# Optimization experiments

Measured on AMD Instinct MI355X. Metric: run time of the kernel, lower is better.

## Reference

```python
import jax, jax.numpy as jnp
import numpy as np

K = 7      # kernel_size
PAD = 3    # padding ('same' with stride 1)
G = 16     # groups


def _unfold(x):
    """torch nn.Unfold equivalent, stride=1, dilation=1.
    Returns [B, C, K*K, H, W] with kernel positions ordered (kh, kw),
    matching torch's (c, kh, kw) channel-major layout after reshape."""
    B, C, H, W = x.shape
    xp = jnp.pad(x, ((0, 0), (0, 0), (PAD, PAD), (PAD, PAD)))
    patches = jnp.stack(
        [xp[:, :, i:i + H, j:j + W] for i in range(K) for j in range(K)],
        axis=2,
    )
    return patches


def setup_inputs() -> dict:
    key = jax.random.key(0)
    k1, k2, k3 = jax.random.split(key, 3)
    B, C, H, W = 4, 256, 64, 64
    x = jax.random.normal(k1, (B, C, H, W), dtype=jnp.float32)
    # 1x1 conv producing kernel_prod*groups = 49*16 = 784 channels (with bias)
    w_kernel = jax.random.normal(k2, (G * K * K, C), dtype=jnp.float32) * 0.05
    b_kernel = jax.random.normal(k3, (G * K * K,), dtype=jnp.float32) * 0.05
    return {"x": x, "w_kernel": w_kernel, "b_kernel": b_kernel}


def reference(x, w_kernel, b_kernel):
    B, C, H, W = x.shape
    Cg = C // G
    # unfolded input: [B, G, C//G, K*K, H, W]
    patches = _unfold(x).reshape(B, G, Cg, K * K, H, W)
    # dynamic per-pixel kernel: AvgPool(k=1) is identity at stride 1,
    # then 1x1 conv with bias -> [B, G*K*K, H, W]
    kern = jnp.einsum('bchw,kc->bkhw', x, w_kernel) + b_kernel[None, :, None, None]
    kern = kern.reshape(B, G, 1, K * K, H, W)
    # multiply and sum-reduce over kernel positions, flatten groups
    out = (patches * kern).sum(axis=3).reshape(B, C, H, W)
    return out
```

## Files before the change

kernel.cpp:

```cpp
#include <hip/hip_runtime.h>


#define B_   4
#define C_   256
#define G_   16
#define KK_  49
#define KS_  7
#define PD_  3

#define PROW  72
#define POCT  (70*PROW)
#define XP8_BYTES (B_*32*POCT*16)
#define WBF_OFF   XP8_BYTES

typedef __attribute__((ext_vector_type(8))) short bf16x8;
typedef __attribute__((ext_vector_type(4))) float f32x4;
typedef unsigned short ushort_t;

__device__ inline unsigned f2bf(float f) {
    unsigned u = __float_as_uint(f);
    u += 0x7FFF + ((u >> 16) & 1);
    return u >> 16;
}

__global__ __launch_bounds__(256)
void cvt_xp8(const float* __restrict__ x, const float* __restrict__ wk,
             ushort_t* __restrict__ xp8, unsigned* __restrict__ wbf) {
    const int t = threadIdx.x;
    if (blockIdx.x == 64) {
        const int slice = blockIdx.z * 4 + blockIdx.y;
        const float2* wk2 = (const float2*)wk;
        const int base = slice * 6272;
        for (int k = t; k < 6272; k += 256) {
            float2 v = wk2[base + k];
            wbf[base + k] = f2bf(v.x) | (f2bf(v.y) << 16);
        }
        return;
    }
    if (blockIdx.x == 65) {
        const int b  = blockIdx.z;
        const int o0 = blockIdx.y * 8;
        const uint4 z = make_uint4(0u, 0u, 0u, 0u);
        for (int e = t; e < 6 * PROW * 8; e += 256) {
            const int o = e / (6 * PROW);
            const int f = e - o * (6 * PROW);
            const int r = f / PROW;
            const int c = f - r * PROW;
            const int row = (r < 3) ? r : 64 + r;
            *(uint4*)(xp8 + ((size_t)((b << 5) + o0 + o) * POCT + row * PROW + c) * 8) = z;
        }
        return;
    }
    __shared__ float tile[64][65];
    const int c0 = blockIdx.y * 64;
    const int b  = blockIdx.z;
    const int px_r = t & 63;
    #pragma unroll
    for (int i = 0; i < 16; ++i) {
        int ch = (t >> 6) + i * 4;
        tile[ch][px_r] = x[((size_t)(b * C_ + c0 + ch) << 12) + blockIdx.x * 64 + px_r];
    }
    __syncthreads();
    const int lane = t & 63;
    const int ob = t >> 6;
    #pragma unroll
    for (int jj = 0; jj < 2; ++jj) {
        const int j = ob + jj * 4;
        ushort_t* rowbase = xp8 + ((size_t)((b << 5) + (c0 >> 3) + j) * POCT
                                   + (blockIdx.x + 3) * PROW) * 8;
        #pragma unroll
        for (int cc = 0; cc < 2; ++cc) {
            const int col = lane + cc * 64;
            if (col < PROW) {
                uint4 v = make_uint4(0u, 0u, 0u, 0u);
                if (col >= 3 && col < 67) {
                    const int p = col - 3;
                    unsigned u[4];
                    #pragma unroll
                    for (int k2 = 0; k2 < 4; ++k2) {
                        float a0 = tile[j * 8 + 2 * k2][p];
                        float a1 = tile[j * 8 + 2 * k2 + 1][p];
                        u[k2] = f2bf(a0) | (f2bf(a1) << 16);
                    }
                    v = make_uint4(u[0], u[1], u[2], u[3]);
                }
                *(uint4*)(rowbase + col * 8) = v;
            }
        }
    }
}

__global__ __launch_bounds__(512, 8)
void inv_fused(const ushort_t* __restrict__ xp8,
               const ushort_t* __restrict__ wbf,
               const float* __restrict__ bk,
               float* __restrict__ out) {
    __shared__ unsigned lds[7168];

    const int bid  = blockIdx.x;
    const int g    = bid >> 6;
    const int b    = (bid >> 4) & 3;
    const int tile = bid & 15;
    const int gy0  = tile * 4;
    const int p0   = tile * 256;

    const int tid  = threadIdx.x;
    const int wv   = tid >> 6;
    const int ln15 = tid & 15;
    const int quad = (tid & 63) >> 4;

    f32x4 acc[8];
    #pragma unroll
    for (int i = 0; i < 8; ++i) acc[i] = (f32x4){0.f, 0.f, 0.f, 0.f};

    const char* bbase = (const char*)xp8 + (size_t)b * 32 * POCT * 16;
    const char* abase = (const char*)wbf + (size_t)g * KK_ * 512;

    int vb0, vb1;
    {
        int gi0 = p0 + wv * 32 + ln15;
        int gi1 = gi0 + 16;
        vb0 = (quad * POCT + ((gi0 >> 6) + 3) * PROW + 3 + (gi0 & 63)) * 16;
        vb1 = (quad * POCT + ((gi1 >> 6) + 3) * PROW + 3 + (gi1 & 63)) * 16;
    }
    int va  = ln15 * 512 + quad * 16;
    const int va3 = 48 * 512 + quad * 16;

    #pragma unroll
    for (int k = 0; k < 8; ++k) {
        bf16x8 af0 = *(const bf16x8*)(abase + va);
        bf16x8 af1 = *(const bf16x8*)(abase + 8192 + va);
        bf16x8 af2 = *(const bf16x8*)(abase + 16384 + va);
        bf16x8 af3 = *(const bf16x8*)(abase + va3 + k * 64);
        bf16x8 bf0 = *(const bf16x8*)(bbase + vb0);
        bf16x8 bf1 = *(const bf16x8*)(bbase + vb1);
        acc[0] = __builtin_amdgcn_mfma_f32_16x16x32_bf16(af0, bf0, acc[0], 0, 0, 0);
        acc[1] = __builtin_amdgcn_mfma_f32_16x16x32_bf16(af0, bf1, acc[1], 0, 0, 0);
        acc[2] = __builtin_amdgcn_mfma_f32_16x16x32_bf16(af1, bf0, acc[2], 0, 0, 0);
        acc[3] = __builtin_amdgcn_mfma_f32_16x16x32_bf16(af1, bf1, acc[3], 0, 0, 0);
        acc[4] = __builtin_amdgcn_mfma_f32_16x16x32_bf16(af2, bf0, acc[4], 0, 0, 0);
        acc[5] = __builtin_amdgcn_mfma_f32_16x16x32_bf16(af2, bf1, acc[5], 0, 0, 0);
        acc[6] = __builtin_amdgcn_mfma_f32_16x16x32_bf16(af3, bf0, acc[6], 0, 0, 0);
        acc[7] = __builtin_amdgcn_mfma_f32_16x16x32_bf16(af3, bf1, acc[7], 0, 0, 0);
        va  += 64;
        vb0 += 4 * POCT * 16; vb1 += 4 * POCT * 16;
    }

    #define HALO_LD(e_) ({                                                     \
        int e = (e_);                                                          \
        int o = (e >= 700) ? 1 : 0;                                            \
        int f = e - o * 700;                                                   \
        int r = f / 70;                                                        \
        int c = f - r * 70;                                                    \
        *(const uint4*)(bbase + ((size_t)(2 * g + o) * POCT                    \
                                 + (gy0 + r) * PROW + c) * 16); })
    uint4 h0 = HALO_LD(tid);
    uint4 h1 = HALO_LD(tid + 512);
    uint4 h2 = (tid < 376) ? HALO_LD(tid + 1024) : make_uint4(0u, 0u, 0u, 0u);

    #pragma unroll
    for (int mt = 0; mt < 3; ++mt) {
        const int m0 = mt * 16 + quad * 4;
        const float b0 = bk[g * KK_ + m0],     b1 = bk[g * KK_ + m0 + 1];
        const float b2 = bk[g * KK_ + m0 + 2], b3 = bk[g * KK_ + m0 + 3];
        const int q7 = mt * 2 + (quad >> 1);
        #pragma unroll
        for (int nt = 0; nt < 2; ++nt) {
            const int p = wv * 32 + nt * 16 + ln15;
            uint2 d;
            d.x = f2bf(acc[mt * 2 + nt][0] + b0) | (f2bf(acc[mt * 2 + nt][1] + b1) << 16);
            d.y = f2bf(acc[mt * 2 + nt][2] + b2) | (f2bf(acc[mt * 2 + nt][3] + b3) << 16);
            *(uint2*)&lds[(q7 * 256 + p) * 4 + (quad & 1) * 2] = d;
        }
    }
    if (quad == 0) {
        const float b48 = bk[g * KK_ + 48];
        #pragma unroll
        for (int nt = 0; nt < 2; ++nt) {
            const int p = wv * 32 + nt * 16 + ln15;
            lds[(6 * 256 + p) * 4] = f2bf(acc[6 + nt][0] + b48);
        }
    }
    __syncthreads();

    const int pix = tid & 255;
    const int ho  = tid >> 8;
    unsigned kd[28];
    #pragma unroll
    for (int q = 0; q < 7; ++q) {
        uint4 h = *(const uint4*)&lds[(q * 256 + pix) * 4];
        kd[4*q] = h.x; kd[4*q+1] = h.y; kd[4*q+2] = h.z; kd[4*q+3] = h.w;
    }
    __syncthreads();

    *(uint4*)&lds[tid * 4] = h0;
    *(uint4*)&lds[(tid + 512) * 4] = h1;
    if (tid < 376) *(uint4*)&lds[(tid + 1024) * 4] = h2;
    __syncthreads();

    const int py = pix >> 6, px = pix & 63;
    const int hbase = (ho * 700 + py * 70 + px) * 4;

    float a[8];
    #pragma unroll
    for (int q = 0; q < 8; ++q) a[q] = 0.f;
    #pragma unroll
    for (int kh = 0; kh < KS_; ++kh) {
        const uint4* hr = (const uint4*)&lds[hbase + kh * 280];
        #pragma unroll
        for (int kw = 0; kw < KS_; ++kw) {
            uint4 hv = hr[kw];
            const int t49 = kh * KS_ + kw;
            unsigned d = kd[t49 >> 1];
            float kk = __uint_as_float((t49 & 1) ? (d & 0xffff0000u) : (d << 16));
            a[0] = fmaf(__uint_as_float(hv.x << 16), kk, a[0]);
            a[1] = fmaf(__uint_as_float(hv.x),       kk, a[1]);
            a[2] = fmaf(__uint_as_float(hv.y << 16), kk, a[2]);
            a[3] = fmaf(__uint_as_float(hv.y),       kk, a[3]);
            a[4] = fmaf(__uint_as_float(hv.z << 16), kk, a[4]);
            a[5] = fmaf(__uint_as_float(hv.z),       kk, a[5]);
            a[6] = fmaf(__uint_as_float(hv.w << 16), kk, a[6]);
            a[7] = fmaf(__uint_as_float(hv.w),       kk, a[7]);
        }
    }
    const size_t o = ((size_t)(b * C_ + g * 16 + ho * 8) << 12) + p0 + pix;
    #pragma unroll
    for (int q = 0; q < 8; ++q)
        out[o + ((size_t)q << 12)] = a[q];
}

extern "C" void kernel_launch(void* const* d_in, const int* in_sizes, int n_in,
                              void* d_out, int out_size, void* d_ws, size_t ws_size,
                              hipStream_t stream) {
    const float* x  = (const float*)d_in[0];
    const float* wk = (const float*)d_in[1];
    const float* bk = (const float*)d_in[2];
    float* o = (float*)d_out;

    ushort_t* xp8 = (ushort_t*)d_ws;
    unsigned* wbf = (unsigned*)((char*)d_ws + WBF_OFF);

    cvt_xp8<<<dim3(66, 4, B_), dim3(256), 0, stream>>>(x, wk, xp8, wbf);
    inv_fused<<<dim3(1024), dim3(512), 0, stream>>>(
        xp8, (const ushort_t*)wbf, bk, o);
}
```

Measured before the change: 114.0 us.

## Split fused involution kernel into separate GEMM and apply kernels via global buffer

The fused kernel is split in two. One kernel runs the MFMA GEMM that produces per-pixel dynamic kernels and writes them as bf16 to a global workspace. A second kernel reads those kernels and computes the 7x7 weighted sum straight from global memory, with no LDS halo staging. This removes the LDS traffic, the barriers and the register pressure of the fused version, and lets each phase use its own launch shape. In exchange it adds an extra launch and a global round trip for the kernel tensor, about 12.8 MB written and read.

```diff
diff --git a/kernel.cpp b/kernel.cpp
--- a/kernel.cpp
+++ b/kernel.cpp
@@ -12,6 +12,7 @@
 #define POCT  (70*PROW)
 #define XP8_BYTES (B_*32*POCT*16)
 #define WBF_OFF   XP8_BYTES
+#define KERN_OFF  (WBF_OFF + 524288)
 
 typedef __attribute__((ext_vector_type(8))) short bf16x8;
 typedef __attribute__((ext_vector_type(4))) float f32x4;
@@ -91,17 +92,14 @@
 }
 
 __global__ __launch_bounds__(512, 8)
-void inv_fused(const ushort_t* __restrict__ xp8,
-               const ushort_t* __restrict__ wbf,
-               const float* __restrict__ bk,
-               float* __restrict__ out) {
-    __shared__ unsigned lds[7168];
-
+void inv_gemm(const ushort_t* __restrict__ xp8,
+              const ushort_t* __restrict__ wbf,
+              const float* __restrict__ bk,
+              unsigned* __restrict__ kg) {
     const int bid  = blockIdx.x;
     const int g    = bid >> 6;
     const int b    = (bid >> 4) & 3;
     const int tile = bid & 15;
-    const int gy0  = tile * 4;
     const int p0   = tile * 256;
 
     const int tid  = threadIdx.x;
@@ -146,18 +144,7 @@
         vb0 += 4 * POCT * 16; vb1 += 4 * POCT * 16;
     }
 
-    #define HALO_LD(e_) ({                                                     \
-        int e = (e_);                                                          \
-        int o = (e >= 700) ? 1 : 0;                                            \
-        int f = e - o * 700;                                                   \
-        int r = f / 70;                                                        \
-        int c = f - r * 70;                                                    \
-        *(const uint4*)(bbase + ((size_t)(2 * g + o) * POCT                    \
-                                 + (gy0 + r) * PROW + c) * 16); })
-    uint4 h0 = HALO_LD(tid);
-    uint4 h1 = HALO_LD(tid + 512);
-    uint4 h2 = (tid < 376) ? HALO_LD(tid + 1024) : make_uint4(0u, 0u, 0u, 0u);
-
+    const int kbg = b * 16 + g;
     #pragma unroll
     for (int mt = 0; mt < 3; ++mt) {
         const int m0 = mt * 16 + quad * 4;
@@ -166,47 +153,53 @@
         const int q7 = mt * 2 + (quad >> 1);
         #pragma unroll
         for (int nt = 0; nt < 2; ++nt) {
-            const int p = wv * 32 + nt * 16 + ln15;
+            const int p = p0 + wv * 32 + nt * 16 + ln15;
             uint2 d;
             d.x = f2bf(acc[mt * 2 + nt][0] + b0) | (f2bf(acc[mt * 2 + nt][1] + b1) << 16);
             d.y = f2bf(acc[mt * 2 + nt][2] + b2) | (f2bf(acc[mt * 2 + nt][3] + b3) << 16);
-            *(uint2*)&lds[(q7 * 256 + p) * 4 + (quad & 1) * 2] = d;
+            *(uint2*)&kg[((((kbg * 7 + q7) << 12) + p) << 2) + (quad & 1) * 2] = d;
         }
     }
     if (quad == 0) {
         const float b48 = bk[g * KK_ + 48];
         #pragma unroll
         for (int nt = 0; nt < 2; ++nt) {
-            const int p = wv * 32 + nt * 16 + ln15;
-            lds[(6 * 256 + p) * 4] = f2bf(acc[6 + nt][0] + b48);
-        }
-    }
-    __syncthreads();
-
-    const int pix = tid & 255;
-    const int ho  = tid >> 8;
+            const int p = p0 + wv * 32 + nt * 16 + ln15;
+            kg[(((kbg * 7 + 6) << 12) + p) << 2] = f2bf(acc[6 + nt][0] + b48);
+        }
+    }
+}
+
+__global__ __launch_bounds__(256, 8)
+void inv_apply(const ushort_t* __restrict__ xp8,
+               const unsigned* __restrict__ kg,
+               float* __restrict__ out) {
+    const int bid = blockIdx.x;
+    const int ho  = bid & 1;
+    const int tq  = (bid >> 1) & 15;
+    const int b   = (bid >> 5) & 3;
+    const int g   = bid >> 7;
+    const int tid = threadIdx.x;
+    const int px  = tq * 256 + tid;
+    const int row = px >> 6, col = px & 63;
+
+    const int kbg = b * 16 + g;
     unsigned kd[28];
     #pragma unroll
     for (int q = 0; q < 7; ++q) {
-        uint4 h = *(const uint4*)&lds[(q * 256 + pix) * 4];
+        uint4 h = *(const uint4*)&kg[(((kbg * 7 + q) << 12) + px) << 2];
         kd[4*q] = h.x; kd[4*q+1] = h.y; kd[4*q+2] = h.z; kd[4*q+3] = h.w;
     }
-    __syncthreads();
-
-    *(uint4*)&lds[tid * 4] = h0;
-    *(uint4*)&lds[(tid + 512) * 4] = h1;
-    if (tid < 376) *(uint4*)&lds[(tid + 1024) * 4] = h2;
-    __syncthreads();
-
-    const int py = pix >> 6, px = pix & 63;
-    const int hbase = (ho * 700 + py * 70 + px) * 4;
+
+    const char* hb = (const char*)xp8
+        + ((size_t)(b * 32 + 2 * g + ho) * POCT + row * PROW + col) * 16;
 
     float a[8];
     #pragma unroll
     for (int q = 0; q < 8; ++q) a[q] = 0.f;
     #pragma unroll
     for (int kh = 0; kh < KS_; ++kh) {
-        const uint4* hr = (const uint4*)&lds[hbase + kh * 280];
+        const uint4* hr = (const uint4*)(hb + (size_t)kh * PROW * 16);
         #pragma unroll
         for (int kw = 0; kw < KS_; ++kw) {
             uint4 hv = hr[kw];
@@ -223,7 +216,7 @@
             a[7] = fmaf(__uint_as_float(hv.w),       kk, a[7]);
         }
     }
-    const size_t o = ((size_t)(b * C_ + g * 16 + ho * 8) << 12) + p0 + pix;
+    const size_t o = ((size_t)(b * C_ + g * 16 + ho * 8) << 12) + px;
     #pragma unroll
     for (int q = 0; q < 8; ++q)
         out[o + ((size_t)q << 12)] = a[q];
@@ -239,8 +232,10 @@
 
     ushort_t* xp8 = (ushort_t*)d_ws;
     unsigned* wbf = (unsigned*)((char*)d_ws + WBF_OFF);
+    unsigned* kg  = (unsigned*)((char*)d_ws + KERN_OFF);
 
     cvt_xp8<<<dim3(66, 4, B_), dim3(256), 0, stream>>>(x, wk, xp8, wbf);
-    inv_fused<<<dim3(1024), dim3(512), 0, stream>>>(
-        xp8, (const ushort_t*)wbf, bk, o);
-}
+    inv_gemm<<<dim3(1024), dim3(512), 0, stream>>>(
+        xp8, (const ushort_t*)wbf, bk, kg);
+    inv_apply<<<dim3(2048), dim3(256), 0, stream>>>(xp8, kg, o);
+}
```

Measured after the change: 131.1 us. 15.0% more time.
